# Kernel tuning notes

Hardware: AMD Instinct MI355X
Metric: run time of the kernel (lower is better)

The kernel has to match this reference:

```python
import jax, jax.numpy as jnp
import numpy as np


def setup_inputs() -> dict:
    key = jax.random.key(0)
    ks = jax.random.split(key, 4)
    B, H, W, C = 4, 64, 64, 256
    d = C // 8
    x = jax.random.normal(ks[0], (B, H, W, C), dtype=jnp.float32)
    # 1x1 conv weights as [C_in, C_out] matrices (Glorot-ish scale)
    Wq = jax.random.normal(ks[1], (C, d), dtype=jnp.float32) * (1.0 / np.sqrt(C))
    Wk = jax.random.normal(ks[2], (C, d), dtype=jnp.float32) * (1.0 / np.sqrt(C))
    Wv = jax.random.normal(ks[3], (C, C), dtype=jnp.float32) * (1.0 / np.sqrt(C))
    bq = jnp.zeros((d,), dtype=jnp.float32)
    bk = jnp.zeros((d,), dtype=jnp.float32)
    bv = jnp.zeros((C,), dtype=jnp.float32)
    gamma = jnp.float32(0.0)  # matches tf.Variable(0.0)
    return {"x": x, "Wq": Wq, "bq": bq, "Wk": Wk, "bk": bk, "Wv": Wv, "bv": bv, "gamma": gamma}


def reference(x, Wq, bq, Wk, bk, Wv, bv, gamma):
    B, H, W, C = x.shape
    N = H * W
    xf = x.reshape(B, N, C)  # spatial tokens
    q = xf @ Wq + bq  # [B, N, d]
    k = xf @ Wk + bk  # [B, N, d]
    v = xf @ Wv + bv  # [B, N, C]
    energy = jnp.einsum("bnd,bmd->bnm", q, k)  # [B, N, N]
    attn = jax.nn.softmax(energy, axis=-1)
    out = jnp.einsum("bnm,bmc->bnc", attn, v).reshape(B, H, W, C)
    return gamma * out + x
```

## Files before the change

kernel.cpp:

```cpp
#include <hip/hip_runtime.h>
#include <hip/hip_bf16.h>

typedef __attribute__((ext_vector_type(8)))  short short8;
typedef __attribute__((ext_vector_type(4)))  float f32x4;
typedef __attribute__((ext_vector_type(16))) float f32x16;
typedef __attribute__((ext_vector_type(4)))  unsigned int u32x4;

#define LOG2E 1.4426950408889634f

static __device__ __forceinline__ unsigned short f2bf(float f) {
    union { float f; unsigned u; } v; v.f = f;
    unsigned r = v.u + 0x7fffu + ((v.u >> 16) & 1u);
    return (unsigned short)(r >> 16);
}
static __device__ __forceinline__ unsigned cvt_pk_bf16(float lo, float hi) {
    unsigned r;
    asm("v_cvt_pk_bf16_f32 %0, %1, %2" : "=v"(r) : "v"(lo), "v"(hi));
    return r;
}
static __device__ __forceinline__ float exp2_hw(float x) {
    float r;
    asm("v_exp_f32 %0, %1" : "=v"(r) : "v"(x));
    return r;
}

__global__ __launch_bounds__(64) void transpose_w(
    const float* __restrict__ Wq, const float* __restrict__ Wk,
    const float* __restrict__ Wv, unsigned short* __restrict__ Wtf)
{
    const int g  = blockIdx.x;
    const int ct = g >> 3, kk = g & 7;
    const int l  = threadIdx.x;
    const int col = ct * 16 + (l & 15);
    const int k0  = kk * 32 + (l >> 4) * 8;
    const float* W; int c, ldw;
    if (col < 32)      { W = Wq; c = col;      ldw = 32;  }
    else if (col < 64) { W = Wk; c = col - 32; ldw = 32;  }
    else               { W = Wv; c = col - 64; ldw = 256; }
    ushort4 o0, o1;
    o0.x = f2bf(W[(size_t)(k0 + 0) * ldw + c]);
    o0.y = f2bf(W[(size_t)(k0 + 1) * ldw + c]);
    o0.z = f2bf(W[(size_t)(k0 + 2) * ldw + c]);
    o0.w = f2bf(W[(size_t)(k0 + 3) * ldw + c]);
    o1.x = f2bf(W[(size_t)(k0 + 4) * ldw + c]);
    o1.y = f2bf(W[(size_t)(k0 + 5) * ldw + c]);
    o1.z = f2bf(W[(size_t)(k0 + 6) * ldw + c]);
    o1.w = f2bf(W[(size_t)(k0 + 7) * ldw + c]);
    *reinterpret_cast<ushort4*>(Wtf + (size_t)g * 512 + l * 8)     = o0;
    *reinterpret_cast<ushort4*>(Wtf + (size_t)g * 512 + l * 8 + 4) = o1;
}

__global__ __launch_bounds__(256) void proj_kernel(
    const float* __restrict__ x, const unsigned short* __restrict__ Wtf,
    const float* __restrict__ bq, const float* __restrict__ bk,
    const float* __restrict__ bv,
    unsigned short* __restrict__ Qb, unsigned short* __restrict__ Kf,
    unsigned short* __restrict__ Vf)
{
    __shared__ unsigned short x_lds[64][264];
    const int tid = threadIdx.x;
    const int M0  = (blockIdx.x >> 1) * 64;
    const int ctb = (blockIdx.x & 1) * 10;

    #pragma unroll
    for (int j = 0; j < 16; ++j) {
        int idx = j * 256 + tid;
        int row = idx >> 6;
        int qc  = idx & 63;
        const float4 v = *reinterpret_cast<const float4*>(x + (size_t)(M0 + row) * 256 + qc * 4);
        ushort4 o;
        o.x = f2bf(v.x); o.y = f2bf(v.y); o.z = f2bf(v.z); o.w = f2bf(v.w);
        *reinterpret_cast<ushort4*>(&x_lds[row][qc * 4]) = o;
    }
    __syncthreads();

    const int w  = tid >> 6;
    const int l  = tid & 63;
    const int lr = l & 15;
    const int lg = l >> 4;

    short8 a[8];
    #pragma unroll
    for (int kk = 0; kk < 8; ++kk)
        a[kk] = *reinterpret_cast<const short8*>(&x_lds[w * 16 + lr][kk * 32 + lg * 8]);

    const int b   = M0 >> 12;
    const int kt  = (M0 & 4095) >> 6;

    for (int ct = ctb; ct < ctb + 10; ++ct) {
        const int col = ct * 16 + lr;
        f32x4 acc = {0.f, 0.f, 0.f, 0.f};
        #pragma unroll
        for (int kk = 0; kk < 8; ++kk) {
            const short8 bfr = *reinterpret_cast<const short8*>(
                Wtf + ((size_t)ct * 8 + kk) * 512 + l * 8);
            acc = __builtin_amdgcn_mfma_f32_16x16x32_bf16(a[kk], bfr, acc, 0, 0, 0);
        }
        const int rbase = M0 + w * 16 + lg * 4;
        if (ct < 2) {
            const float bias = bq[col];
            #pragma unroll
            for (int r = 0; r < 4; ++r)
                Qb[(size_t)(rbase + r) * 32 + col] = f2bf((acc[r] + bias) * LOG2E);
        } else if (ct < 4) {
            const int colp = col - 32;
            const float bias = bk[colp];
            const int dd = colp >> 4, hj = (colp >> 3) & 1, jj = colp & 7;
            #pragma unroll
            for (int r = 0; r < 4; ++r) {
                const int tt = (rbase + r) & 4095;
                const size_t e = (size_t)b * 131072 + (size_t)kt * 2048
                               + (((tt >> 5) & 1) * 2 + dd) * 512
                               + (hj * 32 + (tt & 31)) * 8 + jj;
                Kf[e] = f2bf(acc[r] + bias);
            }
        } else {
            const int colp = col - 64;
            const float bias = bv[colp];
            const int kk_f = w;
            const int hi_v = (lg >> 1) & 1;
            const int j0   = (lg & 1) * 4;
            const size_t e = (size_t)b * 1048576 + (size_t)kt * 16384
                           + (colp >> 5) * 2048 + kk_f * 512
                           + (hi_v * 32 + (colp & 31)) * 8 + j0;
            ushort4 o;
            o.x = f2bf(acc[0] + bias); o.y = f2bf(acc[1] + bias);
            o.z = f2bf(acc[2] + bias); o.w = f2bf(acc[3] + bias);
            *reinterpret_cast<ushort4*>(Vf + e) = o;
        }
    }
}

__global__ __launch_bounds__(128, 2) void attn_kernel(
    const unsigned short* __restrict__ Qb, const unsigned short* __restrict__ Kf,
    const unsigned short* __restrict__ Vf, const float* __restrict__ x,
    const float* __restrict__ gamma_p, float* __restrict__ out)
{
    __shared__ float O_sh[4][16][64];
    __shared__ float l_sh[2][32];

    const int i  = blockIdx.x;
    const int b  = (i & 7) >> 1;
    const int t  = ((i >> 3) << 1) | (i & 1);
    const int qt = t >> 1;
    const int cg = t & 1;

    const int tid = threadIdx.x;
    const int kh  = tid >> 6;
    const int l   = tid & 63;
    const int l5  = l & 31;
    const int hi  = l >> 5;

    const size_t bN = (size_t)b * 4096;
    const int q0 = qt * 32;
    const int c0 = cg * 128;

    const unsigned short* Kfb = Kf + (size_t)b * 131072 + l * 8;
    const unsigned short* Vfb = Vf + (size_t)b * 1048576 + (c0 >> 5) * 2048 + l * 8;

    short8 qb[2];
    #pragma unroll
    for (int dd = 0; dd < 2; ++dd)
        qb[dd] = *reinterpret_cast<const short8*>(
            Qb + (bN + (size_t)(q0 + l5)) * 32 + dd * 16 + hi * 8);

    f32x16 Oa[4];
    #pragma unroll
    for (int ct = 0; ct < 4; ++ct)
        #pragma unroll
        for (int r = 0; r < 16; ++r) Oa[ct][r] = 0.f;
    float ls0 = 0.f, ls1 = 0.f, ls2 = 0.f, ls3 = 0.f;

    f32x16 z;
    #pragma unroll
    for (int r = 0; r < 16; ++r) z[r] = 0.f;

    const int kt0 = kh * 32;

    auto loadK = [&](short8 (&kA)[2][2], int ktg) {
        const unsigned short* kp = Kfb + (size_t)ktg * 2048;
        #pragma unroll
        for (int ks = 0; ks < 2; ++ks)
            #pragma unroll
            for (int dd = 0; dd < 2; ++dd)
                kA[ks][dd] = *reinterpret_cast<const short8*>(kp + (ks * 2 + dd) * 512);
    };
    auto loadV = [&](short8 (&vA)[4][4], int ktg) {
        const unsigned short* vp = Vfb + (size_t)ktg * 16384;
        #pragma unroll
        for (int ct = 0; ct < 4; ++ct)
            #pragma unroll
            for (int kk = 0; kk < 4; ++kk)
                vA[ct][kk] = *reinterpret_cast<const short8*>(vp + ct * 2048 + kk * 512);
    };

    auto body = [&](short8 (&kcur)[2][2], short8 (&knxt)[2][2],
                    short8 (&vcur)[4][4], short8 (&vnxt)[4][4], int ktgn) {
        loadV(vnxt, ktgn);
        loadK(knxt, ktgn);
        f32x16 p0 = __builtin_amdgcn_mfma_f32_32x32x16_bf16(kcur[0][0], qb[0], z, 0, 0, 0);
        f32x16 p1 = __builtin_amdgcn_mfma_f32_32x32x16_bf16(kcur[1][0], qb[0], z, 0, 0, 0);
        p0        = __builtin_amdgcn_mfma_f32_32x32x16_bf16(kcur[0][1], qb[1], p0, 0, 0, 0);
        p1        = __builtin_amdgcn_mfma_f32_32x32x16_bf16(kcur[1][1], qb[1], p1, 0, 0, 0);
        short8 pa[4];
        #pragma unroll
        for (int ks = 0; ks < 2; ++ks) {
            float e[16];
            #pragma unroll
            for (int r = 0; r < 16; ++r) {
                const float s = (ks == 0) ? p0[r] : p1[r];
                e[r] = exp2_hw(s);
                switch (r & 3) {
                    case 0: ls0 += e[r]; break;
                    case 1: ls1 += e[r]; break;
                    case 2: ls2 += e[r]; break;
                    default: ls3 += e[r]; break;
                }
            }
            unsigned c[8];
            #pragma unroll
            for (int n = 0; n < 8; ++n) c[n] = cvt_pk_bf16(e[2 * n], e[2 * n + 1]);
            #pragma unroll
            for (int k2 = 0; k2 < 2; ++k2) {
                unsigned d0 = c[4 * k2 + 0], d2 = c[4 * k2 + 2];
                unsigned d1 = c[4 * k2 + 1], d3 = c[4 * k2 + 3];
                asm("v_permlane32_swap_b32 %0, %1" : "+v"(d0), "+v"(d2));
                asm("v_permlane32_swap_b32 %0, %1" : "+v"(d1), "+v"(d3));
                u32x4 u = {d0, d1, d2, d3};
                pa[ks * 2 + k2] = __builtin_bit_cast(short8, u);
            }
        }
        #pragma unroll
        for (int kk = 0; kk < 4; ++kk)
            #pragma unroll
            for (int ct = 0; ct < 4; ++ct)
                Oa[ct] = __builtin_amdgcn_mfma_f32_32x32x16_bf16(pa[kk], vcur[ct][kk], Oa[ct], 0, 0, 0);
    };

    short8 kA0[2][2], kA1[2][2];
    short8 vA[4][4], vB[4][4];
    loadK(kA0, kt0);
    loadV(vA, kt0);
    for (int kt = 0; kt < 32; kt += 2) {
        body(kA0, kA1, vA, vB, kt0 + kt + 1);
        body(kA1, kA0, vB, vA, kt0 + ((kt + 2) & 31));
    }

    float lsum = (ls0 + ls1) + (ls2 + ls3);
    lsum += __shfl_xor(lsum, 32);
    if (hi == 0) l_sh[kh][l5] = lsum;
    #pragma unroll
    for (int ct = 0; ct < 4; ++ct)
        if ((ct >> 1) != kh) {
            #pragma unroll
            for (int r = 0; r < 16; ++r)
                O_sh[ct][r][hi * 32 + l5] = Oa[ct][r];
        }
    __syncthreads();

    const float gamma = gamma_p[0];
    #pragma unroll
    for (int ct = 0; ct < 4; ++ct)
        if ((ct >> 1) == kh) {
            #pragma unroll
            for (int r = 0; r < 16; ++r) {
                const int qr = (r & 3) + 8 * (r >> 2) + 4 * hi;
                const float ltot = l_sh[0][qr] + l_sh[1][qr];
                const float osum = Oa[ct][r] + O_sh[ct][r][hi * 32 + l5];
                const size_t idx = (bN + (size_t)(q0 + qr)) * 256 + c0 + ct * 32 + l5;
                out[idx] = gamma * (osum / ltot) + x[idx];
            }
        }
}

extern "C" void kernel_launch(void* const* d_in, const int* in_sizes, int n_in,
                              void* d_out, int out_size, void* d_ws, size_t ws_size,
                              hipStream_t stream) {
    const float* x     = (const float*)d_in[0];
    const float* Wq    = (const float*)d_in[1];
    const float* bq    = (const float*)d_in[2];
    const float* Wk    = (const float*)d_in[3];
    const float* bk    = (const float*)d_in[4];
    const float* Wv    = (const float*)d_in[5];
    const float* bv    = (const float*)d_in[6];
    const float* gamma = (const float*)d_in[7];
    float* out = (float*)d_out;

    unsigned short* Qb  = (unsigned short*)d_ws;
    unsigned short* Kf  = Qb + (size_t)16384 * 32;
    unsigned short* Vf  = Kf + (size_t)16384 * 32;
    unsigned short* Wtf = Vf + (size_t)4 * 256 * 4096;

    transpose_w<<<160, 64, 0, stream>>>(Wq, Wk, Wv, Wtf);
    proj_kernel<<<512, 256, 0, stream>>>(x, Wtf, bq, bk, bv, Qb, Kf, Vf);
    attn_kernel<<<1024, 128, 0, stream>>>(Qb, Kf, Vf, x, gamma, out);
}
```

Baseline: 80.05 us.

## Stage K/V tiles into LDS via global_load_lds double buffering

Replaces the register double-buffered K/V global loads with direct global-to-LDS async copies (global_load_lds) into a per-wave double-buffered LDS pool. The tile granularity is halved to 32 keys per step, and fragments are read back from LDS before the MFMAs. This is meant to cut VGPR pressure and overlap loads with compute. The cost is extra LDS traffic and a vmcnt-based wait that relies on per-wave ordering. The epilogue reuses the same pool and adds a barrier.

```diff
diff --git a/kernel.cpp b/kernel.cpp
--- a/kernel.cpp
+++ b/kernel.cpp
@@ -22,6 +22,11 @@
     float r;
     asm("v_exp_f32 %0, %1" : "=v"(r) : "v"(x));
     return r;
+}
+static __device__ __forceinline__ void gll16(const unsigned short* g, unsigned short* lds) {
+    __builtin_amdgcn_global_load_lds(
+        (const __attribute__((address_space(1))) unsigned int*)g,
+        (__attribute__((address_space(3))) unsigned int*)lds, 16, 0, 0);
 }
 
 __global__ __launch_bounds__(64) void transpose_w(
@@ -136,8 +141,8 @@
     const unsigned short* __restrict__ Vf, const float* __restrict__ x,
     const float* __restrict__ gamma_p, float* __restrict__ out)
 {
-    __shared__ float O_sh[4][16][64];
-    __shared__ float l_sh[2][32];
+    __shared__ short8 pool8[2560];
+    unsigned short* pool = (unsigned short*)pool8;
 
     const int i  = blockIdx.x;
     const int b  = (i & 7) >> 1;
@@ -155,8 +160,10 @@
     const int q0 = qt * 32;
     const int c0 = cg * 128;
 
+    unsigned short* myBuf[2] = { pool + kh * 10240, pool + kh * 10240 + 5120 };
+
     const unsigned short* Kfb = Kf + (size_t)b * 131072 + l * 8;
-    const unsigned short* Vfb = Vf + (size_t)b * 1048576 + (c0 >> 5) * 2048 + l * 8;
+    const unsigned short* Vfb = Vf + (size_t)b * 1048576 + (size_t)(c0 >> 5) * 2048 + l * 8;
 
     short8 qb[2];
     #pragma unroll
@@ -175,41 +182,38 @@
     #pragma unroll
     for (int r = 0; r < 16; ++r) z[r] = 0.f;
 
-    const int kt0 = kh * 32;
-
-    auto loadK = [&](short8 (&kA)[2][2], int ktg) {
-        const unsigned short* kp = Kfb + (size_t)ktg * 2048;
-        #pragma unroll
-        for (int ks = 0; ks < 2; ++ks)
-            #pragma unroll
-            for (int dd = 0; dd < 2; ++dd)
-                kA[ks][dd] = *reinterpret_cast<const short8*>(kp + (ks * 2 + dd) * 512);
+    auto stage = [&](int bi, int parity) {
+        const int g64   = kh * 32 + (bi >> 1);
+        const int khalf = bi & 1;
+        const unsigned short* vsrc = Vfb + (size_t)g64 * 16384 + khalf * 1024;
+        unsigned short* dstb = myBuf[parity];
+        #pragma unroll
+        for (int cgl = 0; cgl < 4; ++cgl)
+            #pragma unroll
+            for (int kkl = 0; kkl < 2; ++kkl)
+                gll16(vsrc + cgl * 2048 + kkl * 512, dstb + (cgl * 2 + kkl) * 512);
+        const unsigned short* ksrc = Kfb + (size_t)g64 * 2048 + khalf * 1024;
+        gll16(ksrc,       dstb + 4096);
+        gll16(ksrc + 512, dstb + 4096 + 512);
     };
-    auto loadV = [&](short8 (&vA)[4][4], int ktg) {
-        const unsigned short* vp = Vfb + (size_t)ktg * 16384;
-        #pragma unroll
-        for (int ct = 0; ct < 4; ++ct)
-            #pragma unroll
-            for (int kk = 0; kk < 4; ++kk)
-                vA[ct][kk] = *reinterpret_cast<const short8*>(vp + ct * 2048 + kk * 512);
-    };
-
-    auto body = [&](short8 (&kcur)[2][2], short8 (&knxt)[2][2],
-                    short8 (&vcur)[4][4], short8 (&vnxt)[4][4], int ktgn) {
-        loadV(vnxt, ktgn);
-        loadK(knxt, ktgn);
-        f32x16 p0 = __builtin_amdgcn_mfma_f32_32x32x16_bf16(kcur[0][0], qb[0], z, 0, 0, 0);
-        f32x16 p1 = __builtin_amdgcn_mfma_f32_32x32x16_bf16(kcur[1][0], qb[0], z, 0, 0, 0);
-        p0        = __builtin_amdgcn_mfma_f32_32x32x16_bf16(kcur[0][1], qb[1], p0, 0, 0, 0);
-        p1        = __builtin_amdgcn_mfma_f32_32x32x16_bf16(kcur[1][1], qb[1], p1, 0, 0, 0);
-        short8 pa[4];
-        #pragma unroll
-        for (int ks = 0; ks < 2; ++ks) {
+
+    stage(0, 0);
+    for (int bi = 0; bi < 64; ++bi) {
+        stage((bi + 1) & 63, (bi + 1) & 1);
+        asm volatile("s_waitcnt vmcnt(10)" ::: "memory");
+        __builtin_amdgcn_sched_barrier(0);
+        unsigned short* buf = myBuf[bi & 1];
+
+        const short8 kA0 = *reinterpret_cast<const short8*>(buf + 4096 + l * 8);
+        const short8 kA1 = *reinterpret_cast<const short8*>(buf + 4096 + 512 + l * 8);
+        f32x16 p = __builtin_amdgcn_mfma_f32_32x32x16_bf16(kA0, qb[0], z, 0, 0, 0);
+        p        = __builtin_amdgcn_mfma_f32_32x32x16_bf16(kA1, qb[1], p, 0, 0, 0);
+        short8 pa[2];
+        {
             float e[16];
             #pragma unroll
             for (int r = 0; r < 16; ++r) {
-                const float s = (ks == 0) ? p0[r] : p1[r];
-                e[r] = exp2_hw(s);
+                e[r] = exp2_hw(p[r]);
                 switch (r & 3) {
                     case 0: ls0 += e[r]; break;
                     case 1: ls1 += e[r]; break;
@@ -227,34 +231,31 @@
                 asm("v_permlane32_swap_b32 %0, %1" : "+v"(d0), "+v"(d2));
                 asm("v_permlane32_swap_b32 %0, %1" : "+v"(d1), "+v"(d3));
                 u32x4 u = {d0, d1, d2, d3};
-                pa[ks * 2 + k2] = __builtin_bit_cast(short8, u);
-            }
-        }
-        #pragma unroll
-        for (int kk = 0; kk < 4; ++kk)
-            #pragma unroll
-            for (int ct = 0; ct < 4; ++ct)
-                Oa[ct] = __builtin_amdgcn_mfma_f32_32x32x16_bf16(pa[kk], vcur[ct][kk], Oa[ct], 0, 0, 0);
-    };
-
-    short8 kA0[2][2], kA1[2][2];
-    short8 vA[4][4], vB[4][4];
-    loadK(kA0, kt0);
-    loadV(vA, kt0);
-    for (int kt = 0; kt < 32; kt += 2) {
-        body(kA0, kA1, vA, vB, kt0 + kt + 1);
-        body(kA1, kA0, vB, vA, kt0 + ((kt + 2) & 31));
+                pa[k2] = __builtin_bit_cast(short8, u);
+            }
+        }
+        #pragma unroll
+        for (int kk = 0; kk < 2; ++kk)
+            #pragma unroll
+            for (int ct = 0; ct < 4; ++ct) {
+                const short8 vf = *reinterpret_cast<const short8*>(
+                    buf + (ct * 2 + kk) * 512 + l * 8);
+                Oa[ct] = __builtin_amdgcn_mfma_f32_32x32x16_bf16(pa[kk], vf, Oa[ct], 0, 0, 0);
+            }
     }
 
     float lsum = (ls0 + ls1) + (ls2 + ls3);
     lsum += __shfl_xor(lsum, 32);
-    if (hi == 0) l_sh[kh][l5] = lsum;
+    __syncthreads();
+    float* O_shf = (float*)pool;
+    float* l_shf = (float*)pool + 4096;
+    if (hi == 0) l_shf[kh * 32 + l5] = lsum;
     #pragma unroll
     for (int ct = 0; ct < 4; ++ct)
         if ((ct >> 1) != kh) {
             #pragma unroll
             for (int r = 0; r < 16; ++r)
-                O_sh[ct][r][hi * 32 + l5] = Oa[ct][r];
+                O_shf[(ct * 16 + r) * 64 + hi * 32 + l5] = Oa[ct][r];
         }
     __syncthreads();
 
@@ -265,8 +266,8 @@
             #pragma unroll
             for (int r = 0; r < 16; ++r) {
                 const int qr = (r & 3) + 8 * (r >> 2) + 4 * hi;
-                const float ltot = l_sh[0][qr] + l_sh[1][qr];
-                const float osum = Oa[ct][r] + O_sh[ct][r][hi * 32 + l5];
+                const float ltot = l_shf[qr] + l_shf[32 + qr];
+                const float osum = Oa[ct][r] + O_shf[(ct * 16 + r) * 64 + hi * 32 + l5];
                 const size_t idx = (bN + (size_t)(q0 + qr)) * 256 + c0 + ct * 32 + l5;
                 out[idx] = gamma * (osum / ltot) + x[idx];
             }
```

Measured after the change: 108.4 us. 1.35x slower.
